# Optimization experiments

Measured on AMD Instinct MI355X. Metric: run time of the kernel, lower is better.

Reference implementation:

```python
import jax, jax.numpy as jnp
import numpy as np

BLOCK_SIZE = 128
N_OUT = 4096
K_IN = 4096


def setup_inputs() -> dict:
    key = jax.random.key(0)
    k_x, k_w, k_s = jax.random.split(key, 3)
    x = jax.random.normal(k_x, (1, 1024, K_IN), dtype=jnp.float32)
    # ternary weights stored as int8 in {-2,-1,0,+1} (zero-point subtracted)
    weight_q = (jax.random.randint(k_w, (N_OUT, K_IN), 0, 4) - 2).astype(jnp.int8)
    n_blocks = K_IN // BLOCK_SIZE
    scales = jax.random.uniform(k_s, (N_OUT, n_blocks), dtype=jnp.float32) * 0.1 + 0.01
    return {"x": x, "weight_q": weight_q, "scales": scales}


def reference(x, weight_q, scales):
    N, K = weight_q.shape
    n_blocks = K // BLOCK_SIZE
    orig_shape = x.shape
    # [tokens, n_blocks, block_size]
    x_blocked = x.reshape(-1, n_blocks, BLOCK_SIZE).astype(jnp.float32)
    # [N, n_blocks, block_size]
    w_blocked = weight_q.reshape(N, n_blocks, BLOCK_SIZE).astype(jnp.float32)
    # per-block partial dot products: [tokens, N, n_blocks]
    raw = jnp.einsum('bki,nki->bnk', x_blocked, w_blocked)
    # apply per-(out_feature, block) scale then reduce over blocks
    out = (raw * scales).sum(axis=-1)  # [tokens, N]
    return out.astype(x.dtype).reshape(*orig_shape[:-1], N)
```

## Files before the change

### kernel.cpp

```cpp
#include <hip/hip_runtime.h>
#include <stdint.h>


#define MM 1024
#define NN 4096
#define KK 4096
#define BK 128

typedef __attribute__((ext_vector_type(4))) int intx4;
typedef __attribute__((ext_vector_type(4))) float floatx4;

typedef const __attribute__((address_space(1))) void global_cvoid;
typedef __attribute__((address_space(3))) void lds_void;

__global__ __launch_bounds__(256) void prep(const float* __restrict__ x,
                                            const int* __restrict__ wq,
                                            char* __restrict__ xq,
                                            float* __restrict__ qrow,
                                            char* __restrict__ wb) {
    const int tid = threadIdx.x;
    if (blockIdx.x < MM) {
        const int m = blockIdx.x;
        const float* xr = x + (size_t)m * KK;
        floatx4 v[4];
        float amax = 0.f;
#pragma unroll
        for (int c = 0; c < 4; ++c) {
            v[c] = *(const floatx4*)(xr + (c * 256 + tid) * 4);
#pragma unroll
            for (int e = 0; e < 4; ++e) amax = fmaxf(amax, fabsf(v[c][e]));
        }
#pragma unroll
        for (int off = 32; off; off >>= 1) amax = fmaxf(amax, __shfl_down(amax, off));
        __shared__ float wmax[4];
        if ((tid & 63) == 0) wmax[tid >> 6] = amax;
        __syncthreads();
        amax = fmaxf(fmaxf(wmax[0], wmax[1]), fmaxf(wmax[2], wmax[3]));
        amax = fmaxf(amax, 1e-20f);
        const float qinv = 127.0f / amax;
        if (tid == 0) qrow[m] = amax / 127.0f;
#pragma unroll
        for (int c = 0; c < 4; ++c) {
            int p = 0;
#pragma unroll
            for (int e = 0; e < 4; ++e) {
                float r = rintf(v[c][e] * qinv);
                r = fminf(fmaxf(r, -127.f), 127.f);
                p |= ((int)r & 255) << (8 * e);
            }
            *(int*)(xq + (size_t)m * KK + (c * 256 + tid) * 4) = p;
        }
    } else {
        const int blk = blockIdx.x - MM;
#pragma unroll
        for (int c = 0; c < 4; ++c) {
            size_t c4 = (size_t)blk * 1024 + c * 256 + tid;
            intx4 a = ((const intx4*)wq)[c4];
            ((int*)wb)[c4] = (a[0] & 255) | ((a[1] & 255) << 8) |
                             ((a[2] & 255) << 16) | (a[3] << 24);
        }
    }
}

__global__ __launch_bounds__(256) void q8_gemm(const char* __restrict__ xq,
                                               const char* __restrict__ wb,
                                               const float* __restrict__ qrow,
                                               const float* __restrict__ scales,
                                               float* __restrict__ out) {
    __shared__ char As[2][64 * BK];
    __shared__ char Bs[2][128 * BK];
    __shared__ float Sl[128 * 33];

    const int tid  = threadIdx.x;
    const int lane = tid & 63;
    const int wave = tid >> 6;
    const int r16  = lane & 15;
    const int quad = lane >> 4;
    const int sw   = r16 & 7;
    const int wn   = wave * 32;

    const int bid = blockIdx.x;
    const int xcd = bid & 7, loc = bid >> 3;
    const int nT = xcd * 4 + (loc & 3);
    const int mT = loc >> 2;
    const int mBase = mT * 64, nBase = nT * 128;

    const int rg = lane >> 3;
    const int cs = (lane & 7) ^ rg;
    const char* gA = xq + (size_t)(mBase + wave * 16 + rg) * KK + cs * 16;
    const char* gB = wb + (size_t)(nBase + wave * 32 + rg) * KK + cs * 16;
    const int ldsRowA = wave * 16;
    const int ldsRowB = wave * 32;

    floatx4 facc[4][2];
#pragma unroll
    for (int i = 0; i < 4; ++i)
#pragma unroll
        for (int j = 0; j < 2; ++j) facc[i][j] = (floatx4){0.f, 0.f, 0.f, 0.f};

#define STAGE(BUF, SLAB)                                                        \
    {                                                                           \
        _Pragma("unroll")                                                       \
        for (int t = 0; t < 2; ++t)                                             \
            __builtin_amdgcn_global_load_lds(                                   \
                (global_cvoid*)(gA + (size_t)(t * 8) * KK + (SLAB) * BK),       \
                (lds_void*)&As[BUF][(ldsRowA + t * 8) * BK], 16, 0, 0);         \
        _Pragma("unroll")                                                       \
        for (int t = 0; t < 4; ++t)                                             \
            __builtin_amdgcn_global_load_lds(                                   \
                (global_cvoid*)(gB + (size_t)(t * 8) * KK + (SLAB) * BK),       \
                (lds_void*)&Bs[BUF][(ldsRowB + t * 8) * BK], 16, 0, 0);         \
    }

#define COMPUTE(BUF, SLAB)                                                      \
    {                                                                           \
        float sf0 = Sl[(wn + r16) * 33 + (SLAB)];                               \
        float sf1 = Sl[(wn + 16 + r16) * 33 + (SLAB)];                          \
        intx4 iacc[4][2];                                                       \
        _Pragma("unroll")                                                       \
        for (int kp = 0; kp < 2; ++kp) {                                        \
            intx4 av[4], bv[2];                                                 \
            _Pragma("unroll")                                                   \
            for (int i = 0; i < 4; ++i)                                         \
                av[i] = *(const intx4*)&As[BUF][(i * 16 + r16) * BK +           \
                                               (((kp * 4 + quad) ^ sw) << 4)];  \
            _Pragma("unroll")                                                   \
            for (int j = 0; j < 2; ++j)                                         \
                bv[j] = *(const intx4*)&Bs[BUF][(wn + j * 16 + r16) * BK +      \
                                               (((kp * 4 + quad) ^ sw) << 4)];  \
            _Pragma("unroll")                                                   \
            for (int i = 0; i < 4; ++i)                                         \
                _Pragma("unroll")                                               \
                for (int j = 0; j < 2; ++j)                                     \
                    iacc[i][j] = __builtin_amdgcn_mfma_i32_16x16x64_i8(         \
                        av[i], bv[j], kp ? iacc[i][j] : (intx4){0, 0, 0, 0},    \
                        0, 0, 0);                                               \
        }                                                                       \
        _Pragma("unroll")                                                       \
        for (int i = 0; i < 4; ++i)                                             \
            _Pragma("unroll")                                                   \
            for (int r = 0; r < 4; ++r) {                                       \
                facc[i][0][r] += (float)iacc[i][0][r] * sf0;                    \
                facc[i][1][r] += (float)iacc[i][1][r] * sf1;                    \
            }                                                                   \
    }

    STAGE(0, 0)
    for (int t = tid; t < 4096; t += 256) {
        int nl = t >> 5, b = t & 31;
        Sl[nl * 33 + b] = scales[(size_t)(nBase + nl) * 32 + b];
    }
    __syncthreads();

    const int NIT = KK / BK;
    for (int it = 0; it < NIT; it += 2) {
        if (it + 1 < NIT) STAGE(1, it + 1)
        COMPUTE(0, it)
        __syncthreads();
        if (it + 2 < NIT) STAGE(0, it + 2)
        COMPUTE(1, it + 1)
        __syncthreads();
    }

#pragma unroll
    for (int i = 0; i < 4; ++i) {
        floatx4 qv = *(const floatx4*)(qrow + mBase + i * 16 + quad * 4);
#pragma unroll
        for (int r = 0; r < 4; ++r) {
            int mg = mBase + i * 16 + quad * 4 + r;
            float* orow = out + (size_t)mg * NN + nBase + wn + r16;
#pragma unroll
            for (int j = 0; j < 2; ++j) orow[j * 16] = facc[i][j][r] * qv[r];
        }
    }
#undef STAGE
#undef COMPUTE
}

extern "C" void kernel_launch(void* const* d_in, const int* in_sizes, int n_in,
                              void* d_out, int out_size, void* d_ws, size_t ws_size,
                              hipStream_t stream) {
    const float* x      = (const float*)d_in[0];
    const int*   wq     = (const int*)d_in[1];
    const float* scales = (const float*)d_in[2];
    float*       out    = (float*)d_out;

    char*  xq   = (char*)d_ws;
    float* qrow = (float*)((char*)d_ws + (size_t)MM * KK);
    char*  wb   = (char*)d_ws + (size_t)MM * KK + 4096;

    prep<<<MM + (size_t)NN * KK / 16 / 256, 256, 0, stream>>>(x, wq, xq, qrow, wb);
    q8_gemm<<<(MM / 64) * (NN / 128), 256, 0, stream>>>(xq, wb, qrow, scales, out);
}
```

Measured before the change: 145.8 us.

## Pack ternary weights to 2 bits and unpack into LDS inside GEMM

```diff
diff --git a/kernel.cpp b/kernel.cpp
--- a/kernel.cpp
+++ b/kernel.cpp
@@ -13,11 +13,22 @@
 typedef const __attribute__((address_space(1))) void global_cvoid;
 typedef __attribute__((address_space(3))) void lds_void;
 
+__device__ __forceinline__ intx4 unpack16(unsigned p) {
+    intx4 o;
+#pragma unroll
+    for (int g = 0; g < 4; ++g) {
+        unsigned t = (p >> (8 * g)) & 0xFFu;
+        unsigned s = (t | (t << 6) | (t << 12) | (t << 18)) & 0x03030303u;
+        o[g] = (int)__builtin_amdgcn_perm(0u, 0x0100FFFEu, s);
+    }
+    return o;
+}
+
 __global__ __launch_bounds__(256) void prep(const float* __restrict__ x,
                                             const int* __restrict__ wq,
                                             char* __restrict__ xq,
                                             float* __restrict__ qrow,
-                                            char* __restrict__ wb) {
+                                            unsigned* __restrict__ wp) {
     const int tid = threadIdx.x;
     if (blockIdx.x < MM) {
         const int m = blockIdx.x;
@@ -52,18 +63,26 @@
         }
     } else {
         const int blk = blockIdx.x - MM;
-#pragma unroll
-        for (int c = 0; c < 4; ++c) {
-            size_t c4 = (size_t)blk * 1024 + c * 256 + tid;
-            intx4 a = ((const intx4*)wq)[c4];
-            ((int*)wb)[c4] = (a[0] & 255) | ((a[1] & 255) << 8) |
-                             ((a[2] & 255) << 16) | (a[3] << 24);
+        const int n   = blk * 32 + (tid >> 3);
+        const int c   = tid & 7;
+        const int* wr = wq + (size_t)n * KK + c * 16;
+        for (int slab = 0; slab < 32; ++slab) {
+            const int* p4 = wr + slab * 128;
+            unsigned pk = 0;
+#pragma unroll
+            for (int e = 0; e < 4; ++e) {
+                intx4 a = *(const intx4*)(p4 + e * 4);
+                unsigned b = (unsigned)(((a[0] + 2) & 3) | (((a[1] + 2) & 3) << 2) |
+                                        (((a[2] + 2) & 3) << 4) | (((a[3] + 2) & 3) << 6));
+                pk |= b << (8 * e);
+            }
+            wp[(size_t)slab * (NN * 8) + n * 8 + c] = pk;
         }
     }
 }
 
 __global__ __launch_bounds__(256) void q8_gemm(const char* __restrict__ xq,
-                                               const char* __restrict__ wb,
+                                               const unsigned* __restrict__ wp,
                                                const float* __restrict__ qrow,
                                                const float* __restrict__ scales,
                                                float* __restrict__ out) {
@@ -88,9 +107,11 @@
     const int rg = lane >> 3;
     const int cs = (lane & 7) ^ rg;
     const char* gA = xq + (size_t)(mBase + wave * 16 + rg) * KK + cs * 16;
-    const char* gB = wb + (size_t)(nBase + wave * 32 + rg) * KK + cs * 16;
     const int ldsRowA = wave * 16;
-    const int ldsRowB = wave * 32;
+
+    const unsigned* gBp = wp + (size_t)nBase * 8 + (size_t)tid * 4;
+    const int n_l = tid >> 1;
+    const int cb  = (tid & 1) * 4;
 
     floatx4 facc[4][2];
 #pragma unroll
@@ -98,18 +119,24 @@
 #pragma unroll
         for (int j = 0; j < 2; ++j) facc[i][j] = (floatx4){0.f, 0.f, 0.f, 0.f};
 
-#define STAGE(BUF, SLAB)                                                        \
+#define STAGE_A(BUF, SLAB)                                                      \
     {                                                                           \
         _Pragma("unroll")                                                       \
         for (int t = 0; t < 2; ++t)                                             \
             __builtin_amdgcn_global_load_lds(                                   \
                 (global_cvoid*)(gA + (size_t)(t * 8) * KK + (SLAB) * BK),       \
                 (lds_void*)&As[BUF][(ldsRowA + t * 8) * BK], 16, 0, 0);         \
-        _Pragma("unroll")                                                       \
-        for (int t = 0; t < 4; ++t)                                             \
-            __builtin_amdgcn_global_load_lds(                                   \
-                (global_cvoid*)(gB + (size_t)(t * 8) * KK + (SLAB) * BK),       \
-                (lds_void*)&Bs[BUF][(ldsRowB + t * 8) * BK], 16, 0, 0);         \
+    }
+
+#define LOADB(DST, SLAB) DST = *(const intx4*)(gBp + (size_t)(SLAB) * (NN * 8));
+
+#define UNPACKB(BUF, BP)                                                        \
+    {                                                                           \
+        char* ubase = &Bs[BUF][n_l * 128];                                      \
+        _Pragma("unroll")                                                       \
+        for (int e = 0; e < 4; ++e)                                             \
+            *(intx4*)(ubase + (((cb + e) ^ (n_l & 7)) * 16)) =                  \
+                unpack16((unsigned)BP[e]);                                      \
     }
 
 #define COMPUTE(BUF, SLAB)                                                      \
@@ -145,20 +172,29 @@
             }                                                                   \
     }
 
-    STAGE(0, 0)
+    STAGE_A(0, 0)
+    intx4 bp0;
+    LOADB(bp0, 0)
     for (int t = tid; t < 4096; t += 256) {
         int nl = t >> 5, b = t & 31;
         Sl[nl * 33 + b] = scales[(size_t)(nBase + nl) * 32 + b];
     }
+    UNPACKB(0, bp0)
     __syncthreads();
 
     const int NIT = KK / BK;
     for (int it = 0; it < NIT; it += 2) {
-        if (it + 1 < NIT) STAGE(1, it + 1)
+        intx4 bp1;
+        LOADB(bp1, it + 1)
+        if (it + 1 < NIT) STAGE_A(1, it + 1)
         COMPUTE(0, it)
+        UNPACKB(1, bp1)
         __syncthreads();
-        if (it + 2 < NIT) STAGE(0, it + 2)
+        intx4 bp2;
+        LOADB(bp2, (it + 2) & 31)
+        if (it + 2 < NIT) STAGE_A(0, it + 2)
         COMPUTE(1, it + 1)
+        UNPACKB(0, bp2)
         __syncthreads();
     }
 
@@ -173,7 +209,9 @@
             for (int j = 0; j < 2; ++j) orow[j * 16] = facc[i][j][r] * qv[r];
         }
     }
-#undef STAGE
+#undef STAGE_A
+#undef LOADB
+#undef UNPACKB
 #undef COMPUTE
 }
 
@@ -185,10 +223,10 @@
     const float* scales = (const float*)d_in[2];
     float*       out    = (float*)d_out;
 
-    char*  xq   = (char*)d_ws;
-    float* qrow = (float*)((char*)d_ws + (size_t)MM * KK);
-    char*  wb   = (char*)d_ws + (size_t)MM * KK + 4096;
-
-    prep<<<MM + (size_t)NN * KK / 16 / 256, 256, 0, stream>>>(x, wq, xq, qrow, wb);
-    q8_gemm<<<(MM / 64) * (NN / 128), 256, 0, stream>>>(xq, wb, qrow, scales, out);
-}
+    char*     xq   = (char*)d_ws;
+    float*    qrow = (float*)((char*)d_ws + (size_t)MM * KK);
+    unsigned* wp   = (unsigned*)((char*)d_ws + (size_t)MM * KK + 4096);
+
+    prep<<<MM + NN / 32, 256, 0, stream>>>(x, wq, xq, qrow, wp);
+    q8_gemm<<<(MM / 64) * (NN / 128), 256, 0, stream>>>(xq, wp, qrow, scales, out);
+}
```

Result: slower. 157.0 us (+7.7%).

## Shrink GEMM tile to 64x64 and store block scales as bf16 in LDS

Applied to the files above, without the earlier changes.

```diff
diff --git a/kernel.cpp b/kernel.cpp
--- a/kernel.cpp
+++ b/kernel.cpp
@@ -12,6 +12,15 @@
 
 typedef const __attribute__((address_space(1))) void global_cvoid;
 typedef __attribute__((address_space(3))) void lds_void;
+
+__device__ __forceinline__ unsigned short f2bf(float f) {
+    union { float f; unsigned u; } v; v.f = f;
+    return (unsigned short)((v.u + 0x7FFFu + ((v.u >> 16) & 1u)) >> 16);
+}
+__device__ __forceinline__ float bf2f(unsigned short b) {
+    union { unsigned u; float f; } v; v.u = ((unsigned)b) << 16;
+    return v.f;
+}
 
 __global__ __launch_bounds__(256) void prep(const float* __restrict__ x,
                                             const int* __restrict__ wq,
@@ -68,8 +77,8 @@
                                                const float* __restrict__ scales,
                                                float* __restrict__ out) {
     __shared__ char As[2][64 * BK];
-    __shared__ char Bs[2][128 * BK];
-    __shared__ float Sl[128 * 33];
+    __shared__ char Bs[2][64 * BK];
+    __shared__ unsigned short Sl[64 * 33];
 
     const int tid  = threadIdx.x;
     const int lane = tid & 63;
@@ -77,26 +86,23 @@
     const int r16  = lane & 15;
     const int quad = lane >> 4;
     const int sw   = r16 & 7;
-    const int wn   = wave * 32;
+    const int wn   = wave * 16;
 
     const int bid = blockIdx.x;
     const int xcd = bid & 7, loc = bid >> 3;
-    const int nT = xcd * 4 + (loc & 3);
-    const int mT = loc >> 2;
-    const int mBase = mT * 64, nBase = nT * 128;
+    const int nT = xcd * 8 + (loc & 7);
+    const int mT = loc >> 3;
+    const int mBase = mT * 64, nBase = nT * 64;
 
     const int rg = lane >> 3;
     const int cs = (lane & 7) ^ rg;
     const char* gA = xq + (size_t)(mBase + wave * 16 + rg) * KK + cs * 16;
-    const char* gB = wb + (size_t)(nBase + wave * 32 + rg) * KK + cs * 16;
-    const int ldsRowA = wave * 16;
-    const int ldsRowB = wave * 32;
+    const char* gB = wb + (size_t)(nBase + wave * 16 + rg) * KK + cs * 16;
+    const int ldsRow = wave * 16;
 
-    floatx4 facc[4][2];
+    floatx4 facc[4];
 #pragma unroll
-    for (int i = 0; i < 4; ++i)
-#pragma unroll
-        for (int j = 0; j < 2; ++j) facc[i][j] = (floatx4){0.f, 0.f, 0.f, 0.f};
+    for (int i = 0; i < 4; ++i) facc[i] = (floatx4){0.f, 0.f, 0.f, 0.f};
 
 #define STAGE(BUF, SLAB)                                                        \
     {                                                                           \
@@ -104,51 +110,43 @@
         for (int t = 0; t < 2; ++t)                                             \
             __builtin_amdgcn_global_load_lds(                                   \
                 (global_cvoid*)(gA + (size_t)(t * 8) * KK + (SLAB) * BK),       \
-                (lds_void*)&As[BUF][(ldsRowA + t * 8) * BK], 16, 0, 0);         \
+                (lds_void*)&As[BUF][(ldsRow + t * 8) * BK], 16, 0, 0);          \
         _Pragma("unroll")                                                       \
-        for (int t = 0; t < 4; ++t)                                             \
+        for (int t = 0; t < 2; ++t)                                             \
             __builtin_amdgcn_global_load_lds(                                   \
                 (global_cvoid*)(gB + (size_t)(t * 8) * KK + (SLAB) * BK),       \
-                (lds_void*)&Bs[BUF][(ldsRowB + t * 8) * BK], 16, 0, 0);         \
+                (lds_void*)&Bs[BUF][(ldsRow + t * 8) * BK], 16, 0, 0);          \
     }
 
 #define COMPUTE(BUF, SLAB)                                                      \
     {                                                                           \
-        float sf0 = Sl[(wn + r16) * 33 + (SLAB)];                               \
-        float sf1 = Sl[(wn + 16 + r16) * 33 + (SLAB)];                          \
-        intx4 iacc[4][2];                                                       \
+        float sf = bf2f(Sl[(wn + r16) * 33 + (SLAB)]);                          \
+        intx4 iacc[4];                                                          \
         _Pragma("unroll")                                                       \
         for (int kp = 0; kp < 2; ++kp) {                                        \
-            intx4 av[4], bv[2];                                                 \
+            intx4 av[4], bv;                                                    \
             _Pragma("unroll")                                                   \
             for (int i = 0; i < 4; ++i)                                         \
                 av[i] = *(const intx4*)&As[BUF][(i * 16 + r16) * BK +           \
                                                (((kp * 4 + quad) ^ sw) << 4)];  \
-            _Pragma("unroll")                                                   \
-            for (int j = 0; j < 2; ++j)                                         \
-                bv[j] = *(const intx4*)&Bs[BUF][(wn + j * 16 + r16) * BK +      \
-                                               (((kp * 4 + quad) ^ sw) << 4)];  \
+            bv = *(const intx4*)&Bs[BUF][(wn + r16) * BK +                      \
+                                         (((kp * 4 + quad) ^ sw) << 4)];        \
             _Pragma("unroll")                                                   \
             for (int i = 0; i < 4; ++i)                                         \
-                _Pragma("unroll")                                               \
-                for (int j = 0; j < 2; ++j)                                     \
-                    iacc[i][j] = __builtin_amdgcn_mfma_i32_16x16x64_i8(         \
-                        av[i], bv[j], kp ? iacc[i][j] : (intx4){0, 0, 0, 0},    \
-                        0, 0, 0);                                               \
+                iacc[i] = __builtin_amdgcn_mfma_i32_16x16x64_i8(                \
+                    av[i], bv, kp ? iacc[i] : (intx4){0, 0, 0, 0}, 0, 0, 0);    \
         }                                                                       \
         _Pragma("unroll")                                                       \
         for (int i = 0; i < 4; ++i)                                             \
             _Pragma("unroll")                                                   \
-            for (int r = 0; r < 4; ++r) {                                       \
-                facc[i][0][r] += (float)iacc[i][0][r] * sf0;                    \
-                facc[i][1][r] += (float)iacc[i][1][r] * sf1;                    \
-            }                                                                   \
+            for (int r = 0; r < 4; ++r)                                         \
+                facc[i][r] += (float)iacc[i][r] * sf;                           \
     }
 
     STAGE(0, 0)
-    for (int t = tid; t < 4096; t += 256) {
+    for (int t = tid; t < 2048; t += 256) {
         int nl = t >> 5, b = t & 31;
-        Sl[nl * 33 + b] = scales[(size_t)(nBase + nl) * 32 + b];
+        Sl[nl * 33 + b] = f2bf(scales[(size_t)(nBase + nl) * 32 + b]);
     }
     __syncthreads();
 
@@ -168,9 +166,7 @@
 #pragma unroll
         for (int r = 0; r < 4; ++r) {
             int mg = mBase + i * 16 + quad * 4 + r;
-            float* orow = out + (size_t)mg * NN + nBase + wn + r16;
-#pragma unroll
-            for (int j = 0; j < 2; ++j) orow[j * 16] = facc[i][j][r] * qv[r];
+            out[(size_t)mg * NN + nBase + wn + r16] = facc[i][r] * qv[r];
         }
     }
 #undef STAGE
@@ -190,5 +186,5 @@
     char*  wb   = (char*)d_ws + (size_t)MM * KK + 4096;
 
     prep<<<MM + (size_t)NN * KK / 16 / 256, 256, 0, stream>>>(x, wq, xq, qrow, wb);
-    q8_gemm<<<(MM / 64) * (NN / 128), 256, 0, stream>>>(xq, wb, qrow, scales, out);
+    q8_gemm<<<(MM / 64) * (NN / 64), 256, 0, stream>>>(xq, wb, qrow, scales, out);
 }
```

Measured after the change: 244.2 us. 67.4% more time.
